# Performance work log

Hardware: AMD Instinct MI355X
Metric: run time of the kernel (lower is better)

The kernel has to match this reference:

```python
import jax, jax.numpy as jnp
import numpy as np

NUM_ORI = 16
DEGREE = 2
NUM_LAYERS = 2
LN_EPS = 1e-6


def ori_grid_s1(n):
    theta = jnp.linspace(0.0, 2.0 * jnp.pi, n + 1)[:-1]
    return jnp.stack([jnp.cos(theta), jnp.sin(theta)], axis=-1)  # (O, 2)


def poly_feats(z, degree):
    # PolynomialFeatures: [z, z*z outer, (z*z)*z outer ...] flattened
    feats = [z]
    p = z
    for _ in range(degree):
        p = (p[..., :, None] * z[..., None, :]).reshape(*z.shape[:-1], -1)
        feats.append(p)
    return jnp.concatenate(feats, axis=-1)


def basis_mlp(z, W1, b1, W2, b2):
    return jax.nn.gelu(jax.nn.gelu(z @ W1 + b1) @ W2 + b2)


def layer_norm(h, scale, bias):
    mu = h.mean(axis=-1, keepdims=True)
    var = ((h - mu) ** 2).mean(axis=-1, keepdims=True)
    return (h - mu) * jax.lax.rsqrt(var + LN_EPS) * scale + bias


def setup_inputs() -> dict:
    key = jax.random.key(0)
    ks = jax.random.split(key, 16)
    B, N, NIN, H, BD, WF, OUT, L = 1, 256, 3, 64, 32, 4, 3, NUM_LAYERS
    s = 0.05
    return {
        'pos': jax.random.normal(ks[0], (B, N, 2), jnp.float32),
        'x': jax.random.normal(ks[1], (B, N, NIN), jnp.float32),
        'skb_W1': jax.random.normal(ks[2], (14, H), jnp.float32) * s,
        'skb_b1': jnp.zeros((H,), jnp.float32),
        'skb_W2': jax.random.normal(ks[3], (H, BD), jnp.float32) * s,
        'skb_b2': jnp.zeros((BD,), jnp.float32),
        'rkb_W1': jax.random.normal(ks[4], (3, H), jnp.float32) * s,
        'rkb_b1': jnp.zeros((H,), jnp.float32),
        'rkb_W2': jax.random.normal(ks[5], (H, BD), jnp.float32) * s,
        'rkb_b2': jnp.zeros((BD,), jnp.float32),
        'emb_W': jax.random.normal(ks[6], (NIN, H), jnp.float32) * s,
        'conv_sW': jax.random.normal(ks[7], (L, BD, H), jnp.float32) * s,
        'conv_rW': jax.random.normal(ks[8], (L, BD, H), jnp.float32) * s,
        'conv_b': jnp.zeros((L, H), jnp.float32),
        'ln_scale': jnp.ones((L, H), jnp.float32),
        'ln_bias': jnp.zeros((L, H), jnp.float32),
        'lin1_W': jax.random.normal(ks[9], (L, H, WF * H), jnp.float32) * s,
        'lin1_b': jnp.zeros((L, WF * H), jnp.float32),
        'lin2_W': jax.random.normal(ks[10], (L, WF * H, H), jnp.float32) * s,
        'lin2_b': jnp.zeros((L, H), jnp.float32),
        'readout_W': jax.random.normal(ks[11], (H, OUT), jnp.float32) * s,
    }


def reference(pos, x, skb_W1, skb_b1, skb_W2, skb_b2, rkb_W1, rkb_b1, rkb_W2, rkb_b2,
              emb_W, conv_sW, conv_rW, conv_b, ln_scale, ln_bias,
              lin1_W, lin1_b, lin2_W, lin2_b, readout_W):
    ori = ori_grid_s1(NUM_ORI)  # (O, 2)
    # rel_pos: (B, n, m, 1, 2) -> broadcast against ori (O, 2)
    rel_pos = pos[:, None, :, None, :] - pos[:, :, None, None, :]
    inv1 = jnp.sum(rel_pos * ori[None, None, None, :, :], axis=-1, keepdims=True)  # (B,N,N,O,1)
    inv2 = jnp.linalg.norm(rel_pos - rel_pos * inv1, axis=-1, keepdims=True)       # (B,N,N,O,1)
    spatial_inv = jnp.concatenate([inv1, inv2], axis=-1)                            # (B,N,N,O,2)
    orient_inv = jnp.sum(ori[:, None, :] * ori[None, :, :], axis=-1, keepdims=True) # (O,O,1)

    kernel_basis = basis_mlp(poly_feats(spatial_inv, DEGREE), skb_W1, skb_b1, skb_W2, skb_b2)  # (B,N,N,O,BD)
    fiber_basis = basis_mlp(poly_feats(orient_inv, DEGREE), rkb_W1, rkb_b1, rkb_W2, rkb_b2)    # (O,O,BD)

    h = x @ emb_W                                  # (B,N,H)
    O = NUM_ORI
    h = jnp.broadcast_to(h[:, :, None, :], (h.shape[0], h.shape[1], O, h.shape[2]))  # (B,N,O,H)

    for i in range(NUM_LAYERS):
        inp = h
        sk = kernel_basis @ conv_sW[i]             # (B,N,N,O,H)
        rk = fiber_basis @ conv_rW[i]              # (O,O,H)
        c = jnp.einsum('bnoc,bmnoc->bmoc', h, sk)  # spatial aggregation
        c = jnp.einsum('bmoc,poc->bmpc', c, rk)    # orientation mixing
        c = c + conv_b[i]
        c = layer_norm(c, ln_scale[i], ln_bias[i])
        c = jax.nn.gelu(c @ lin1_W[i] + lin1_b[i]) @ lin2_W[i] + lin2_b[i]
        h = inp + c

    readout = h @ readout_W                        # (B,N,O,OUT)
    out_scalar = readout.mean(axis=-2)             # (B,N,OUT)
    out_scalar = jnp.sum(out_scalar, axis=1) / out_scalar.shape[1]  # global pool -> (B,OUT)
    return out_scalar
```

## Files before the change

kernel.cpp:

```cpp
#include <hip/hip_runtime.h>
#include <math.h>

#define NPTS 256
#define NORI 16
#define CH   64
#define BD   32
#define HID  64
#define STEP16 0.39269908169872414f

typedef __bf16 bf16x8 __attribute__((ext_vector_type(8)));
typedef float  f32x4  __attribute__((ext_vector_type(4)));

#define MFMA16(a, b, cc) __builtin_amdgcn_mfma_f32_16x16x32_bf16(a, b, cc, 0, 0, 0)

__device__ __forceinline__ float gelu_f(float x) {
    float x2 = x * x;
    float y2 = x * fmaf(0.07135481627f, x2, 1.5957691216f);
    float e = __expf(y2);
    return x - x * __builtin_amdgcn_rcpf(e + 1.0f);
}

__device__ __forceinline__ unsigned pk2(float x, float y) {
    union { __bf16 h[2]; unsigned u; } r;
    r.h[0] = (__bf16)x; r.h[1] = (__bf16)y;
    return r.u;
}

__device__ __forceinline__ void dev_prep(
    const float* __restrict__ skb_W1, const float* __restrict__ skb_W2,
    const float* __restrict__ conv_sW,
    __bf16* __restrict__ w1T, __bf16* __restrict__ w2T, __bf16* __restrict__ w2Tlo,
    __bf16* __restrict__ sWT, __bf16* __restrict__ sWTlo, int t)
{
    if (t < 64) {
        float f[9];
        f[0] = skb_W1[t];
        f[1] = skb_W1[64 + t];
        f[2] = skb_W1[128 + t];
        f[3] = skb_W1[192 + t] + skb_W1[256 + t];
        f[4] = skb_W1[320 + t];
        f[5] = skb_W1[384 + t];
        f[6] = skb_W1[448 + t] + skb_W1[512 + t] + skb_W1[640 + t];
        f[7] = skb_W1[576 + t] + skb_W1[704 + t] + skb_W1[768 + t];
        f[8] = skb_W1[832 + t];
#pragma unroll
        for (int k = 0; k < 9; ++k) {
            __bf16 hi = (__bf16)f[k];
            w1T[t * 32 + k]      = hi;
            w1T[t * 32 + 9 + k]  = (__bf16)(f[k] - (float)hi);
            w1T[t * 32 + 18 + k] = hi;
        }
#pragma unroll
        for (int k = 27; k < 32; ++k) w1T[t * 32 + k] = (__bf16)0.0f;
    }
    for (int i = t; i < 2048; i += 256) {
        int n = i >> 6, kk = i & 63;
        float v = skb_W2[kk * 32 + n];
        __bf16 hi = (__bf16)v;
        w2T[i]   = hi;
        w2Tlo[i] = (__bf16)(v - (float)hi);
    }
    for (int i = t; i < 4096; i += 256) {
        int ll = i >> 11, chh = (i >> 5) & 63, k = i & 31;
        float v = conv_sW[(ll * 32 + k) * 64 + chh];
        __bf16 hi = (__bf16)v;
        sWT[i]   = hi;
        sWTlo[i] = (__bf16)(v - (float)hi);
    }
}

__device__ __forceinline__ void dev_fiber(
    const float* __restrict__ rkb_W1, const float* __restrict__ rkb_b1,
    const float* __restrict__ rkb_W2, const float* __restrict__ rkb_b2,
    const float* __restrict__ conv_rW, float* __restrict__ rk, int p, int t)
{
    __shared__ float w1L[3 * 64], b1L[64], w2L[64 * 32], b2L[32];
    __shared__ float rwL[2 * 32 * 64];
    __shared__ float t1L[16 * 64];
    __shared__ float fbL[16 * 32];

    if (t < 192) w1L[t] = rkb_W1[t];
    if (t >= 192 && t < 256) b1L[t - 192] = rkb_b1[t - 192];
    for (int i = t; i < 2048; i += 256) w2L[i] = rkb_W2[i];
    if (t < 32) b2L[t] = rkb_b2[t];
    for (int i = t; i < 4096; i += 256) rwL[i] = conv_rW[i];
    __syncthreads();

    const int o = t & 15;
    const float cp = cosf(p * STEP16), sp = sinf(p * STEP16);
    const float co = cosf(o * STEP16), so = sinf(o * STEP16);
    const float s0 = cp * co + sp * so;
    const float m1 = s0 * s0, m2 = m1 * s0;

    {
        const int jg = t >> 4;
#pragma unroll
        for (int u = 0; u < 4; ++u) {
            const int j = jg * 4 + u;
            float a = b1L[j] + s0 * w1L[j] + m1 * w1L[64 + j] + m2 * w1L[128 + j];
            t1L[o * 64 + j] = gelu_f(a);
        }
    }
    __syncthreads();
    {
        const int kg = t >> 4;
#pragma unroll
        for (int kk = 0; kk < 2; ++kk) {
            const int k = kg + kk * 16;
            float a = b2L[k];
#pragma unroll
            for (int j = 0; j < 64; ++j) a += t1L[o * 64 + j] * w2L[j * 32 + k];
            fbL[o * 32 + k] = gelu_f(a);
        }
    }
    __syncthreads();
    {
        const int o2 = t >> 4;
        const int chg = (t & 15) * 4;
#pragma unroll
        for (int l = 0; l < 2; ++l) {
            f32x4 acc = {0.f, 0.f, 0.f, 0.f};
#pragma unroll
            for (int k = 0; k < 32; ++k) {
                const float fv = fbL[o2 * 32 + k];
                const f32x4 rv = *(const f32x4*)(rwL + (l * 32 + k) * 64 + chg);
                acc[0] = fmaf(fv, rv[0], acc[0]);
                acc[1] = fmaf(fv, rv[1], acc[1]);
                acc[2] = fmaf(fv, rv[2], acc[2]);
                acc[3] = fmaf(fv, rv[3], acc[3]);
            }
            *(f32x4*)(rk + (l * 256 + p * 16 + o2) * 64 + chg) = acc;
        }
    }
}

__global__ __launch_bounds__(256) void k_prep(
    const float* __restrict__ skb_W1, const float* __restrict__ skb_W2,
    const float* __restrict__ conv_sW,
    __bf16* __restrict__ w1T, __bf16* __restrict__ w2T, __bf16* __restrict__ w2Tlo,
    __bf16* __restrict__ sWT, __bf16* __restrict__ sWTlo)
{
    dev_prep(skb_W1, skb_W2, conv_sW, w1T, w2T, w2Tlo, sWT, sWTlo, threadIdx.x);
}

__global__ __launch_bounds__(256) void k_fiber2(
    const float* __restrict__ rkb_W1, const float* __restrict__ rkb_b1,
    const float* __restrict__ rkb_W2, const float* __restrict__ rkb_b2,
    const float* __restrict__ conv_rW, float* __restrict__ rk)
{
    dev_fiber(rkb_W1, rkb_b1, rkb_W2, rkb_b2, conv_rW, rk, blockIdx.x, threadIdx.x);
}

__global__ __launch_bounds__(256) void k_init(
    const float* __restrict__ x, const float* __restrict__ emb_W, float* __restrict__ h)
{
    int idx = blockIdx.x * 256 + threadIdx.x;
    int ch = idx & 63;
    int n  = idx >> 10;
    h[idx] = x[n * 3] * emb_W[ch] + x[n * 3 + 1] * emb_W[64 + ch] + x[n * 3 + 2] * emb_W[128 + ch];
}

__global__ __launch_bounds__(256) void k_setup(
    const float* __restrict__ x, const float* __restrict__ emb_W, float* __restrict__ h2,
    const float* __restrict__ rkb_W1, const float* __restrict__ rkb_b1,
    const float* __restrict__ rkb_W2, const float* __restrict__ rkb_b2,
    const float* __restrict__ conv_rW, float* __restrict__ rk,
    const float* __restrict__ skb_W1, const float* __restrict__ skb_W2,
    const float* __restrict__ conv_sW,
    __bf16* __restrict__ w1T, __bf16* __restrict__ w2T, __bf16* __restrict__ w2Tlo,
    __bf16* __restrict__ sWT, __bf16* __restrict__ sWTlo)
{
    const int b = blockIdx.x, t = threadIdx.x;
    if (b < 1024) {
        int idx = b * 256 + t;
        int ch = (idx >> 4) & 63;
        int n  = idx >> 10;
        h2[idx] = x[n * 3] * emb_W[ch] + x[n * 3 + 1] * emb_W[64 + ch]
                + x[n * 3 + 2] * emb_W[128 + ch];
    } else if (b < 1040) {
        dev_fiber(rkb_W1, rkb_b1, rkb_W2, rkb_b2, conv_rW, rk, b - 1024, t);
    } else {
        dev_prep(skb_W1, skb_W2, conv_sW, w1T, w2T, w2Tlo, sWT, sWTlo, t);
    }
}

__global__ __launch_bounds__(256) void k_kb2(
    const float* __restrict__ pos,
    const float* __restrict__ skb_b1, const float* __restrict__ skb_b2,
    const __bf16* __restrict__ w1T, const __bf16* __restrict__ w2T,
    const __bf16* __restrict__ w2Tlo, __bf16* __restrict__ kb_g)
{
    const int t = threadIdx.x;
    const int c = t & 15, qq = (t >> 4) & 3, w = t >> 6;
    const int pair = blockIdx.x >> 1, ohalf = blockIdx.x & 1;
    const int m0 = (pair >> 4) * 16, n0 = (pair & 15) * 16;

    bf16x8 w1B[4], w2A[2][2], w2Alo[2][2];
    float b1x[4][4], b2x[2][4];
#pragma unroll
    for (int ni = 0; ni < 4; ++ni) {
        w1B[ni] = *(const bf16x8*)(w1T + (ni * 16 + c) * 32 + qq * 8);
#pragma unroll
        for (int r = 0; r < 4; ++r) b1x[ni][r] = skb_b1[ni * 16 + qq * 4 + r];
    }
#pragma unroll
    for (int mk = 0; mk < 2; ++mk) {
#pragma unroll
        for (int ks = 0; ks < 2; ++ks) {
            w2A[mk][ks]   = *(const bf16x8*)(w2T   + (mk * 16 + c) * 64 + ks * 32 + qq * 8);
            w2Alo[mk][ks] = *(const bf16x8*)(w2Tlo + (mk * 16 + c) * 64 + ks * 32 + qq * 8);
        }
#pragma unroll
        for (int r = 0; r < 4; ++r) b2x[mk][r] = skb_b2[mk * 16 + qq * 4 + r];
    }

    const int n = n0 + c;
    const float pnx = pos[2 * n], pny = pos[2 * n + 1];
    float cosv[4], sinv[4];
#pragma unroll
    for (int oi = 0; oi < 4; ++oi) {
        float th = (float)(ohalf * 4 + oi) * STEP16;
        cosv[oi] = cosf(th); sinv[oi] = sinf(th);
    }
    const int s0lane = c + ((qq & 1) << 5);
    const int s1lane = s0lane + 16;
    const int selhi = qq >> 1;
    const f32x4 zf = {0.f, 0.f, 0.f, 0.f};

#pragma unroll 1
    for (int mi = 0; mi < 4; ++mi) {
        const int m = m0 + w * 4 + mi;
        const float dx = pnx - pos[2 * m];
        const float dy = pny - pos[2 * m + 1];
#pragma unroll
        for (int oi = 0; oi < 4; ++oi) {
            const int o = ohalf * 4 + oi;
            float a = dx * cosv[oi] + dy * sinv[oi];
            float vx = dx - dx * a, vy = dy - dy * a;
            float b = sqrtf(vx * vx + vy * vy);
            float mfv[9];
            mfv[0] = a; mfv[1] = b; mfv[2] = a * a; mfv[3] = a * b; mfv[4] = b * b;
            mfv[5] = mfv[2] * a; mfv[6] = mfv[2] * b; mfv[7] = mfv[3] * b; mfv[8] = mfv[4] * b;
            __bf16 mh[9], ml[9];
#pragma unroll
            for (int i = 0; i < 9; ++i) {
                mh[i] = (__bf16)mfv[i];
                ml[i] = (__bf16)(mfv[i] - (float)mh[i]);
            }
            bf16x8 mb;
            if (qq == 0) {
                mb[0]=mh[0]; mb[1]=mh[1]; mb[2]=mh[2]; mb[3]=mh[3];
                mb[4]=mh[4]; mb[5]=mh[5]; mb[6]=mh[6]; mb[7]=mh[7];
            } else if (qq == 1) {
                mb[0]=mh[8]; mb[1]=mh[0]; mb[2]=mh[1]; mb[3]=mh[2];
                mb[4]=mh[3]; mb[5]=mh[4]; mb[6]=mh[5]; mb[7]=mh[6];
            } else if (qq == 2) {
                mb[0]=mh[7]; mb[1]=mh[8]; mb[2]=ml[0]; mb[3]=ml[1];
                mb[4]=ml[2]; mb[5]=ml[3]; mb[6]=ml[4]; mb[7]=ml[5];
            } else {
                mb[0]=ml[6]; mb[1]=ml[7]; mb[2]=ml[8]; mb[3]=(__bf16)0.0f;
                mb[4]=(__bf16)0.0f; mb[5]=(__bf16)0.0f; mb[6]=(__bf16)0.0f; mb[7]=(__bf16)0.0f;
            }

            unsigned t1p[4][2];
#pragma unroll
            for (int ni = 0; ni < 4; ++ni) {
                f32x4 acc = MFMA16(w1B[ni], mb, zf);
                float g0 = gelu_f(acc[0] + b1x[ni][0]);
                float g1 = gelu_f(acc[1] + b1x[ni][1]);
                float g2 = gelu_f(acc[2] + b1x[ni][2]);
                float g3 = gelu_f(acc[3] + b1x[ni][3]);
                t1p[ni][0] = pk2(g0, g1);
                t1p[ni][1] = pk2(g2, g3);
            }

            bf16x8 B2[2];
#pragma unroll
            for (int ks = 0; ks < 2; ++ks) {
                const unsigned lo0 = t1p[ks * 2][0],     lo1 = t1p[ks * 2][1];
                const unsigned hi0 = t1p[ks * 2 + 1][0], hi1 = t1p[ks * 2 + 1][1];
                unsigned aL0 = (unsigned)__shfl((int)lo0, s0lane);
                unsigned aL1 = (unsigned)__shfl((int)lo1, s0lane);
                unsigned aL2 = (unsigned)__shfl((int)lo0, s1lane);
                unsigned aL3 = (unsigned)__shfl((int)lo1, s1lane);
                unsigned aH0 = (unsigned)__shfl((int)hi0, s0lane);
                unsigned aH1 = (unsigned)__shfl((int)hi1, s0lane);
                unsigned aH2 = (unsigned)__shfl((int)hi0, s1lane);
                unsigned aH3 = (unsigned)__shfl((int)hi1, s1lane);
                union { unsigned u[4]; bf16x8 v; } bu;
                bu.u[0] = selhi ? aH0 : aL0;
                bu.u[1] = selhi ? aH1 : aL1;
                bu.u[2] = selhi ? aH2 : aL2;
                bu.u[3] = selhi ? aH3 : aL3;
                B2[ks] = bu.v;
            }

            const size_t ptP = (size_t)((m * 256 + n) * 16 + o);
            const size_t ptM = (size_t)((n * 256 + m) * 16 + (o ^ 8));
#pragma unroll
            for (int mk = 0; mk < 2; ++mk) {
                f32x4 acc = MFMA16(w2A[mk][0], B2[0], zf);
                acc = MFMA16(w2A[mk][1], B2[1], acc);
                acc = MFMA16(w2Alo[mk][0], B2[0], acc);
                acc = MFMA16(w2Alo[mk][1], B2[1], acc);
                float g0 = gelu_f(acc[0] + b2x[mk][0]);
                float g1 = gelu_f(acc[1] + b2x[mk][1]);
                float g2 = gelu_f(acc[2] + b2x[mk][2]);
                float g3 = gelu_f(acc[3] + b2x[mk][3]);
                uint2 pv; pv.x = pk2(g0, g1); pv.y = pk2(g2, g3);
                const int off = mk * 32 + qq * 8;
                *(uint2*)((char*)kb_g + ptP * 64 + off) = pv;
                *(uint2*)((char*)kb_g + ptM * 64 + off) = pv;
            }
        }
    }
}

__global__ __launch_bounds__(1024) void k_conv2(
    const __bf16* __restrict__ kb_g,
    const __bf16* __restrict__ sWT, const __bf16* __restrict__ sWTlo,
    const float* __restrict__ conv_b, const float* __restrict__ rkg,
    const float* __restrict__ ln_scale, const float* __restrict__ ln_bias,
    const float* __restrict__ lin1_W, const float* __restrict__ lin1_b,
    const float* __restrict__ lin2_W, const float* __restrict__ lin2_b,
    const float* __restrict__ h_in, float* __restrict__ h_out, int l)
{
    __shared__ __align__(16) unsigned char smem[90112];
    const int t = threadIdx.x;
    const int m = blockIdx.x;
    const int w = t >> 6, lane = t & 63;
    const int qq = lane >> 4, c = lane & 15;
    const f32x4 zf = {0.f, 0.f, 0.f, 0.f};

    bf16x8 sWB[4], sWBlo[4];
#pragma unroll
    for (int ni = 0; ni < 4; ++ni) {
        sWB[ni]   = *(const bf16x8*)(sWT   + l * 2048 + (ni * 16 + c) * 32 + qq * 8);
        sWBlo[ni] = *(const bf16x8*)(sWTlo + l * 2048 + (ni * 16 + c) * 32 + qq * 8);
    }

    f32x4 cacc[4];
#pragma unroll
    for (int ni = 0; ni < 4; ++ni)
#pragma unroll
        for (int r = 0; r < 4; ++r) cacc[ni][r] = 0.f;

    const __bf16* kbm = kb_g + ((size_t)m << 17);
    const __bf16* abase = kbm + (size_t)(w * 16 + c) * 32 + qq * 8;

    bf16x8 aF = *(const bf16x8*)(abase);
    f32x4 hc0, hc1, hc2, hc3;
    {
        const float* hp = h_in + (w) * 1024 + c * 16 + qq * 4;
        hc0 = *(const f32x4*)(hp);
        hc1 = *(const f32x4*)(hp + 256);
        hc2 = *(const f32x4*)(hp + 512);
        hc3 = *(const f32x4*)(hp + 768);
    }

#pragma unroll 1
    for (int tile = 0; tile < 16; ++tile) {
        const int tn = (tile < 15) ? tile + 1 : 15;
        bf16x8 aN = *(const bf16x8*)(abase + (size_t)tn * 8192);
        const float* hpn = h_in + (tn * 16 + w) * 1024 + c * 16 + qq * 4;
        f32x4 hn0 = *(const f32x4*)(hpn);
        f32x4 hn1 = *(const f32x4*)(hpn + 256);
        f32x4 hn2 = *(const f32x4*)(hpn + 512);
        f32x4 hn3 = *(const f32x4*)(hpn + 768);

        f32x4 g;
        g = MFMA16(aF, sWB[0], zf);
        g = MFMA16(aF, sWBlo[0], g);
#pragma unroll
        for (int r = 0; r < 4; ++r) cacc[0][r] = fmaf(g[r], hc0[r], cacc[0][r]);
        g = MFMA16(aF, sWB[1], zf);
        g = MFMA16(aF, sWBlo[1], g);
#pragma unroll
        for (int r = 0; r < 4; ++r) cacc[1][r] = fmaf(g[r], hc1[r], cacc[1][r]);
        g = MFMA16(aF, sWB[2], zf);
        g = MFMA16(aF, sWBlo[2], g);
#pragma unroll
        for (int r = 0; r < 4; ++r) cacc[2][r] = fmaf(g[r], hc2[r], cacc[2][r]);
        g = MFMA16(aF, sWB[3], zf);
        g = MFMA16(aF, sWBlo[3], g);
#pragma unroll
        for (int r = 0; r < 4; ++r) cacc[3][r] = fmaf(g[r], hc3[r], cacc[3][r]);

        aF = aN;
        hc0 = hn0; hc1 = hn1; hc2 = hn2; hc3 = hn3;
    }

    {
        float* c1p = (float*)smem;
#pragma unroll
        for (int ni = 0; ni < 4; ++ni)
#pragma unroll
            for (int r = 0; r < 4; ++r)
                c1p[w * 1024 + (qq * 4 + r) * 64 + ni * 16 + c] = cacc[ni][r];
    }
    __syncthreads();
    {
        float* c1p = (float*)smem;
        float* c1r = (float*)(smem + 65536);
        float s = 0.f;
#pragma unroll
        for (int ww = 0; ww < 16; ++ww) s += c1p[ww * 1024 + t];
        c1r[t] = s;
    }
    __syncthreads();

    {
        float* c1r = (float*)(smem + 65536);
        float* cns = (float*)(smem + 69632);
        const int ch = lane;
        const float cb  = conv_b[l * 64 + ch];
        const float lsc = ln_scale[l * 64 + ch], lbi = ln_bias[l * 64 + ch];
        const float* rkp = rkg + (l * 256 + w * 16) * 64 + ch;
        float s = cb;
#pragma unroll
        for (int o = 0; o < 16; ++o) s += c1r[o * 64 + ch] * rkp[o * 64];
        float red = s;
#pragma unroll
        for (int off = 32; off > 0; off >>= 1) red += __shfl_xor(red, off);
        float mu = red * (1.0f / 64.0f);
        float d = s - mu;
        float r2 = d * d;
#pragma unroll
        for (int off = 32; off > 0; off >>= 1) r2 += __shfl_xor(r2, off);
        cns[w * 64 + ch] = d * rsqrtf(r2 * (1.0f / 64.0f) + 1e-6f) * lsc + lbi;
    }
    __syncthreads();

    {
        float* cns = (float*)(smem + 69632);
        float* usS = (float*)(smem + 73728);
        const int j = t & 255, q4 = t >> 8;
        const float* W1l = lin1_W + l * 64 * 256;
        const float bl1 = lin1_b[l * 256 + j];
        float ua[4];
#pragma unroll
        for (int pi = 0; pi < 4; ++pi) ua[pi] = bl1;
#pragma unroll 4
        for (int c2 = 0; c2 < 64; ++c2) {
            const float wv = W1l[c2 * 256 + j];
#pragma unroll
            for (int pi = 0; pi < 4; ++pi)
                ua[pi] = fmaf(cns[(q4 * 4 + pi) * 64 + c2], wv, ua[pi]);
        }
#pragma unroll
        for (int pi = 0; pi < 4; ++pi) usS[(q4 * 4 + pi) * 256 + j] = gelu_f(ua[pi]);
    }
    __syncthreads();

    {
        float* usS = (float*)(smem + 73728);
        const int ch2 = t & 63, pg = t >> 6;
        const float* W2l = lin2_W + l * 256 * 64;
        float o0 = lin2_b[l * 64 + ch2];
#pragma unroll 4
        for (int j = 0; j < 256; ++j)
            o0 = fmaf(usS[pg * 256 + j], W2l[j * 64 + ch2], o0);
        const int i0 = m * 1024 + ch2 * 16 + pg;
        h_out[i0] = h_in[i0] + o0;
    }
}

__global__ __launch_bounds__(512, 1) void k_layer2(
    const float* __restrict__ pos,
    const float* __restrict__ skb_b1, const float* __restrict__ skb_b2,
    const __bf16* __restrict__ w1T, const __bf16* __restrict__ w2T,
    const __bf16* __restrict__ w2Tlo,
    const __bf16* __restrict__ sWT, const __bf16* __restrict__ sWTlo,
    const float* __restrict__ conv_b, const float* __restrict__ rkg,
    const float* __restrict__ ln_scale, const float* __restrict__ ln_bias,
    const float* __restrict__ lin1_W, const float* __restrict__ lin1_b,
    const float* __restrict__ lin2_W, const float* __restrict__ lin2_b,
    const float* __restrict__ h_in, float* __restrict__ h_out, int l)
{
    __shared__ __align__(16) unsigned char smem[57344];
    const int t = threadIdx.x;
    const int m = blockIdx.x;
    const int w = t >> 6, lane = t & 63;
    const int qq = lane >> 4, c = lane & 15;

    bf16x8 w1B[4], sWB[4], sWBlo[4], w2B[2][2], w2Blo[2][2];
    float b1v[4], b2v[2];
#pragma unroll
    for (int ni = 0; ni < 4; ++ni) {
        w1B[ni]   = *(const bf16x8*)(w1T + (ni * 16 + c) * 32 + qq * 8);
        sWB[ni]   = *(const bf16x8*)(sWT   + l * 2048 + (ni * 16 + c) * 32 + qq * 8);
        sWBlo[ni] = *(const bf16x8*)(sWTlo + l * 2048 + (ni * 16 + c) * 32 + qq * 8);
        b1v[ni] = skb_b1[ni * 16 + c];
    }
#pragma unroll
    for (int nt = 0; nt < 2; ++nt) {
        b2v[nt] = skb_b2[nt * 16 + c];
#pragma unroll
        for (int ks = 0; ks < 2; ++ks) {
            w2B[nt][ks]   = *(const bf16x8*)(w2T   + (nt * 16 + c) * 64 + ks * 32 + qq * 8);
            w2Blo[nt][ks] = *(const bf16x8*)(w2Tlo + (nt * 16 + c) * 64 + ks * 32 + qq * 8);
        }
    }

    const float pmx = pos[2 * m], pmy = pos[2 * m + 1];
    float co_ = 0.f, so_ = 0.f;
    if (t < 256) { float th = (float)(t & 15) * STEP16; co_ = cosf(th); so_ = sinf(th); }

    f32x4 cacc[4];
#pragma unroll
    for (int ni = 0; ni < 4; ++ni)
#pragma unroll
        for (int r = 0; r < 4; ++r) cacc[ni][r] = 0.f;

#pragma unroll 1
    for (int tile = 0; tile < 16; ++tile) {
        if (t < 256) {
            const int n = tile * 16 + (t >> 4);
            float dx = pos[2 * n] - pmx, dy = pos[2 * n + 1] - pmy;
            float a = dx * co_ + dy * so_;
            float vx = dx - dx * a, vy = dy - dy * a;
            float b = sqrtf(vx * vx + vy * vy);
            float mf[9];
            mf[0] = a; mf[1] = b; mf[2] = a * a; mf[3] = a * b; mf[4] = b * b;
            mf[5] = mf[2] * a; mf[6] = mf[2] * b; mf[7] = mf[3] * b; mf[8] = mf[4] * b;
            __bf16 s[32];
#pragma unroll
            for (int i = 0; i < 9; ++i) {
                __bf16 hi = (__bf16)mf[i];
                s[i] = hi; s[9 + i] = hi;
                s[18 + i] = (__bf16)(mf[i] - (float)hi);
            }
#pragma unroll
            for (int i = 27; i < 32; ++i) s[i] = (__bf16)0.0f;
            unsigned char* rowp = smem + t * 64;
#pragma unroll
            for (int u = 0; u < 4; ++u) {
                bf16x8 vv;
#pragma unroll
                for (int j = 0; j < 8; ++j) vv[j] = s[u * 8 + j];
                *(bf16x8*)(rowp + ((u ^ (t & 3)) << 4)) = vv;
            }
        }
        __syncthreads();

#pragma unroll
        for (int mm = 0; mm < 2; ++mm) {
            const int row = (2 * w + mm) * 16 + c;
            bf16x8 aF = *(const bf16x8*)(smem + row * 64 + ((qq ^ (row & 3)) << 4));
#pragma unroll
            for (int ni = 0; ni < 4; ++ni) {
                f32x4 acc = {0.f, 0.f, 0.f, 0.f};
                acc = MFMA16(aF, w1B[ni], acc);
#pragma unroll
                for (int r = 0; r < 4; ++r) {
                    const int ro = (2 * w + mm) * 16 + qq * 4 + r;
                    float g = gelu_f(acc[r] + b1v[ni]);
                    const int chc = ni * 16 + c;
                    *(__bf16*)(smem + 16384 + ro * 128 + (((chc >> 3) ^ (ro & 7)) << 4)
                               + ((chc & 7) << 1)) = (__bf16)g;
                }
            }
        }
        __syncthreads();

#pragma unroll
        for (int mm = 0; mm < 2; ++mm) {
            const int row = (2 * w + mm) * 16 + c;
            bf16x8 a0 = *(const bf16x8*)(smem + 16384 + row * 128 + ((qq ^ (row & 7)) << 4));
            bf16x8 a1 = *(const bf16x8*)(smem + 16384 + row * 128 + (((4 + qq) ^ (row & 7)) << 4));
#pragma unroll
            for (int nt = 0; nt < 2; ++nt) {
                f32x4 acc = {0.f, 0.f, 0.f, 0.f};
                acc = MFMA16(a0, w2B[nt][0], acc);
                acc = MFMA16(a1, w2B[nt][1], acc);
                acc = MFMA16(a0, w2Blo[nt][0], acc);
                acc = MFMA16(a1, w2Blo[nt][1], acc);
#pragma unroll
                for (int r = 0; r < 4; ++r) {
                    const int ro = (2 * w + mm) * 16 + qq * 4 + r;
                    float g = gelu_f(acc[r] + b2v[nt]);
                    const int kc = nt * 16 + c;
                    *(__bf16*)(smem + ro * 64 + (((kc >> 3) ^ (ro & 3)) << 4)
                               + ((kc & 7) << 1)) = (__bf16)g;
                }
            }
        }
        __syncthreads();

#pragma unroll
        for (int mm = 0; mm < 2; ++mm) {
            const int mi = 2 * w + mm;
            const int row = mi * 16 + c;
            bf16x8 aF = *(const bf16x8*)(smem + row * 64 + ((qq ^ (row & 3)) << 4));
            const int nbase = (tile * 16 + mi) * 1024 + qq * 256;
#pragma unroll
            for (int ni = 0; ni < 4; ++ni) {
                f32x4 g3 = {0.f, 0.f, 0.f, 0.f};
                g3 = MFMA16(aF, sWB[ni], g3);
                g3 = MFMA16(aF, sWBlo[ni], g3);
#pragma unroll
                for (int r = 0; r < 4; ++r) {
                    float hv = h_in[nbase + r * 64 + ni * 16 + c];
                    cacc[ni][r] = fmaf(g3[r], hv, cacc[ni][r]);
                }
            }
        }
        __syncthreads();
    }

    {
        float* c1p = (float*)smem;
#pragma unroll
        for (int ni = 0; ni < 4; ++ni)
#pragma unroll
            for (int r = 0; r < 4; ++r)
                c1p[w * 1024 + (qq * 4 + r) * 64 + ni * 16 + c] = cacc[ni][r];
    }
    __syncthreads();
    {
        float* c1p = (float*)smem;
        float* c1r = (float*)(smem + 32768);
        for (int i = t; i < 1024; i += 512) {
            float s = 0.f;
#pragma unroll
            for (int ww = 0; ww < 8; ++ww) s += c1p[ww * 1024 + i];
            c1r[i] = s;
        }
    }
    __syncthreads();

    {
        float* c1r = (float*)(smem + 32768);
        float* cns = (float*)(smem + 36864);
        const int ch = lane;
        const float cb  = conv_b[l * 64 + ch];
        const float lsc = ln_scale[l * 64 + ch], lbi = ln_bias[l * 64 + ch];
#pragma unroll
        for (int pp = 0; pp < 2; ++pp) {
            const int p = w + pp * 8;
            const float* rkp = rkg + (l * 256 + p * 16) * 64 + ch;
            float s = cb;
#pragma unroll
            for (int o = 0; o < 16; ++o) s += c1r[o * 64 + ch] * rkp[o * 64];
            float red = s;
#pragma unroll
            for (int off = 32; off > 0; off >>= 1) red += __shfl_xor(red, off);
            float mu = red * (1.0f / 64.0f);
            float d = s - mu;
            float r2 = d * d;
#pragma unroll
            for (int off = 32; off > 0; off >>= 1) r2 += __shfl_xor(r2, off);
            cns[p * 64 + ch] = d * rsqrtf(r2 * (1.0f / 64.0f) + 1e-6f) * lsc + lbi;
        }
    }
    __syncthreads();

    {
        float* cns = (float*)(smem + 36864);
        float* usS = (float*)(smem + 40960);
        const int j = t & 255, half = t >> 8;
        const float* W1l = lin1_W + l * 64 * 256;
        const float bl1 = lin1_b[l * 256 + j];
        float ua[8];
#pragma unroll
        for (int pi = 0; pi < 8; ++pi) ua[pi] = bl1;
#pragma unroll 1
        for (int c2 = 0; c2 < 64; ++c2) {
            const float wv = W1l[c2 * 256 + j];
#pragma unroll
            for (int pi = 0; pi < 8; ++pi)
                ua[pi] = fmaf(cns[(half * 8 + pi) * 64 + c2], wv, ua[pi]);
        }
#pragma unroll
        for (int pi = 0; pi < 8; ++pi) usS[(half * 8 + pi) * 256 + j] = gelu_f(ua[pi]);
    }
    __syncthreads();

    {
        float* usS = (float*)(smem + 40960);
        const int ch2 = t & 63, pg = t >> 6;
        const float* W2l = lin2_W + l * 256 * 64;
        const float bl2 = lin2_b[l * 64 + ch2];
        float o0 = bl2, o1 = bl2;
#pragma unroll 2
        for (int j = 0; j < 256; ++j) {
            const float wv = W2l[j * 64 + ch2];
            o0 = fmaf(usS[pg * 256 + j], wv, o0);
            o1 = fmaf(usS[(pg + 8) * 256 + j], wv, o1);
        }
        const int i0 = (m * 16 + pg) * 64 + ch2;
        const int i1 = (m * 16 + pg + 8) * 64 + ch2;
        h_out[i0] = h_in[i0] + o0;
        h_out[i1] = h_in[i1] + o1;
    }
}

__global__ __launch_bounds__(256) void k_readout_part(
    const float* __restrict__ h, float* __restrict__ part16)
{
    __shared__ float part[4][64];
    const int t = threadIdx.x, b = blockIdx.x;
    const int c = t & 63, seg = t >> 6;
    float s = 0.f;
    const int r0 = b * 256 + seg * 64;
    for (int r = r0; r < r0 + 64; ++r) s += h[r * 64 + c];
    part[seg][c] = s;
    __syncthreads();
    if (t < 64) part16[b * 64 + t] = part[0][t] + part[1][t] + part[2][t] + part[3][t];
}

__global__ __launch_bounds__(256) void k_readout_part2(
    const float* __restrict__ h, float* __restrict__ part16)
{
    const int t = threadIdx.x, b = blockIdx.x;
    const int ch = t >> 2, oq = t & 3;
    float s = 0.f;
#pragma unroll
    for (int nn = 0; nn < 16; ++nn) {
        const int n = b * 16 + nn;
        f32x4 v = *(const f32x4*)(h + n * 1024 + ch * 16 + oq * 4);
        s += (v[0] + v[1]) + (v[2] + v[3]);
    }
    s += __shfl_xor(s, 1);
    s += __shfl_xor(s, 2);
    if (oq == 0) part16[b * 64 + ch] = s;
}

__global__ __launch_bounds__(64) void k_readout_final(
    const float* __restrict__ part16, const float* __restrict__ rW, float* __restrict__ out)
{
    __shared__ float hbar[64];
    const int t = threadIdx.x;
    float s = 0.f;
#pragma unroll
    for (int b = 0; b < 16; ++b) s += part16[b * 64 + t];
    hbar[t] = s * (1.0f / 4096.0f);
    __syncthreads();
    if (t < 3) {
        float s2 = 0.f;
#pragma unroll
        for (int k = 0; k < 64; ++k) s2 += hbar[k] * rW[k * 3 + t];
        out[t] = s2;
    }
}

extern "C" void kernel_launch(void* const* d_in, const int* in_sizes, int n_in,
                              void* d_out, int out_size, void* d_ws, size_t ws_size,
                              hipStream_t stream)
{
    const float* pos      = (const float*)d_in[0];
    const float* x        = (const float*)d_in[1];
    const float* skb_W1   = (const float*)d_in[2];
    const float* skb_b1   = (const float*)d_in[3];
    const float* skb_W2   = (const float*)d_in[4];
    const float* skb_b2   = (const float*)d_in[5];
    const float* rkb_W1   = (const float*)d_in[6];
    const float* rkb_b1   = (const float*)d_in[7];
    const float* rkb_W2   = (const float*)d_in[8];
    const float* rkb_b2   = (const float*)d_in[9];
    const float* emb_W    = (const float*)d_in[10];
    const float* conv_sW  = (const float*)d_in[11];
    const float* conv_rW  = (const float*)d_in[12];
    const float* conv_b   = (const float*)d_in[13];
    const float* ln_scale = (const float*)d_in[14];
    const float* ln_bias  = (const float*)d_in[15];
    const float* lin1_W   = (const float*)d_in[16];
    const float* lin1_b   = (const float*)d_in[17];
    const float* lin2_W   = (const float*)d_in[18];
    const float* lin2_b   = (const float*)d_in[19];
    const float* readout_W= (const float*)d_in[20];
    float* out = (float*)d_out;

    unsigned char* ws = (unsigned char*)d_ws;
    float*  h_a    = (float*)(ws);
    float*  h_b    = (float*)(ws + 1048576);
    float*  rkw    = (float*)(ws + 2097152);
    __bf16* w1T    = (__bf16*)(ws + 2228224);
    __bf16* w2T    = (__bf16*)(ws + 2232320);
    __bf16* w2Tlo  = (__bf16*)(ws + 2236416);
    __bf16* sWT    = (__bf16*)(ws + 2240512);
    __bf16* sWTlo  = (__bf16*)(ws + 2248704);
    float*  part16 = (float*)(ws + 2256896);
    __bf16* kb_g   = (__bf16*)(ws + 2260992);

    const bool fast = (ws_size >= 2260992ull + 67108864ull);

    if (fast) {
        k_setup<<<1041, 256, 0, stream>>>(x, emb_W, h_a,
                                          rkb_W1, rkb_b1, rkb_W2, rkb_b2, conv_rW, rkw,
                                          skb_W1, skb_W2, conv_sW,
                                          w1T, w2T, w2Tlo, sWT, sWTlo);
        k_kb2<<<512, 256, 0, stream>>>(pos, skb_b1, skb_b2, w1T, w2T, w2Tlo, kb_g);
        k_conv2<<<256, 1024, 0, stream>>>(kb_g, sWT, sWTlo, conv_b, rkw,
                                          ln_scale, ln_bias, lin1_W, lin1_b,
                                          lin2_W, lin2_b, h_a, h_b, 0);
        k_conv2<<<256, 1024, 0, stream>>>(kb_g, sWT, sWTlo, conv_b, rkw,
                                          ln_scale, ln_bias, lin1_W, lin1_b,
                                          lin2_W, lin2_b, h_b, h_a, 1);
        k_readout_part2<<<16, 256, 0, stream>>>(h_a, part16);
        k_readout_final<<<1, 64, 0, stream>>>(part16, readout_W, out);
    } else {
        k_prep<<<1, 256, 0, stream>>>(skb_W1, skb_W2, conv_sW, w1T, w2T, w2Tlo, sWT, sWTlo);
        k_fiber2<<<16, 256, 0, stream>>>(rkb_W1, rkb_b1, rkb_W2, rkb_b2, conv_rW, rkw);
        k_init<<<1024, 256, 0, stream>>>(x, emb_W, h_a);
        k_layer2<<<256, 512, 0, stream>>>(pos, skb_b1, skb_b2, w1T, w2T, w2Tlo, sWT, sWTlo,
                                          conv_b, rkw, ln_scale, ln_bias, lin1_W, lin1_b,
                                          lin2_W, lin2_b, h_a, h_b, 0);
        k_layer2<<<256, 512, 0, stream>>>(pos, skb_b1, skb_b2, w1T, w2T, w2Tlo, sWT, sWTlo,
                                          conv_b, rkw, ln_scale, ln_bias, lin1_W, lin1_b,
                                          lin2_W, lin2_b, h_b, h_a, 1);
        k_readout_part<<<16, 256, 0, stream>>>(h_a, part16);
        k_readout_final<<<1, 64, 0, stream>>>(part16, readout_W, out);
    }
}
```

Baseline: 146.3 us.

## Stage kernel-basis tiles into LDS via async global_load_lds with swizzled layout

The conv kernel now streams each 16KB kernel-basis tile into a double-buffered LDS region with async global-to-LDS loads and reads MFMA operands from LDS, synchronising once per tile. The kernel-basis producer writes its output with an XOR swizzle on 16-byte chunks so the LDS reads avoid bank conflicts. It also splits the m range across twice as many blocks for more parallelism. The cost is an extra block-wide barrier per tile and a layout coupling between producer and consumer.

```diff
diff --git a/kernel.cpp b/kernel.cpp
--- a/kernel.cpp
+++ b/kernel.cpp
@@ -12,6 +12,9 @@
 typedef float  f32x4  __attribute__((ext_vector_type(4)));
 
 #define MFMA16(a, b, cc) __builtin_amdgcn_mfma_f32_16x16x32_bf16(a, b, cc, 0, 0, 0)
+#define GLOAD_LDS16(g, l) \
+    __builtin_amdgcn_global_load_lds((const __attribute__((address_space(1))) unsigned int*)(g), \
+                                     (__attribute__((address_space(3))) unsigned int*)(l), 16, 0, 0)
 
 __device__ __forceinline__ float gelu_f(float x) {
     float x2 = x * x;
@@ -192,7 +195,10 @@
 {
     const int t = threadIdx.x;
     const int c = t & 15, qq = (t >> 4) & 3, w = t >> 6;
-    const int pair = blockIdx.x >> 1, ohalf = blockIdx.x & 1;
+    const int b = blockIdx.x;
+    const int pair = b >> 2;
+    const int ohalf = (b >> 1) & 1;
+    const int mhalf = b & 1;
     const int m0 = (pair >> 4) * 16, n0 = (pair & 15) * 16;
 
     bf16x8 w1B[4], w2A[2][2], w2Alo[2][2];
@@ -228,8 +234,8 @@
     const f32x4 zf = {0.f, 0.f, 0.f, 0.f};
 
 #pragma unroll 1
-    for (int mi = 0; mi < 4; ++mi) {
-        const int m = m0 + w * 4 + mi;
+    for (int mi2 = 0; mi2 < 2; ++mi2) {
+        const int m = m0 + w * 4 + mhalf * 2 + mi2;
         const float dx = pnx - pos[2 * m];
         const float dy = pny - pos[2 * m + 1];
 #pragma unroll
@@ -237,10 +243,10 @@
             const int o = ohalf * 4 + oi;
             float a = dx * cosv[oi] + dy * sinv[oi];
             float vx = dx - dx * a, vy = dy - dy * a;
-            float b = sqrtf(vx * vx + vy * vy);
+            float b2 = sqrtf(vx * vx + vy * vy);
             float mfv[9];
-            mfv[0] = a; mfv[1] = b; mfv[2] = a * a; mfv[3] = a * b; mfv[4] = b * b;
-            mfv[5] = mfv[2] * a; mfv[6] = mfv[2] * b; mfv[7] = mfv[3] * b; mfv[8] = mfv[4] * b;
+            mfv[0] = a; mfv[1] = b2; mfv[2] = a * a; mfv[3] = a * b2; mfv[4] = b2 * b2;
+            mfv[5] = mfv[2] * a; mfv[6] = mfv[2] * b2; mfv[7] = mfv[3] * b2; mfv[8] = mfv[4] * b2;
             __bf16 mh[9], ml[9];
 #pragma unroll
             for (int i = 0; i < 9; ++i) {
@@ -297,6 +303,7 @@
 
             const size_t ptP = (size_t)((m * 256 + n) * 16 + o);
             const size_t ptM = (size_t)((n * 256 + m) * 16 + (o ^ 8));
+            const int swz = o & 3;
 #pragma unroll
             for (int mk = 0; mk < 2; ++mk) {
                 f32x4 acc = MFMA16(w2A[mk][0], B2[0], zf);
@@ -308,7 +315,7 @@
                 float g2 = gelu_f(acc[2] + b2x[mk][2]);
                 float g3 = gelu_f(acc[3] + b2x[mk][3]);
                 uint2 pv; pv.x = pk2(g0, g1); pv.y = pk2(g2, g3);
-                const int off = mk * 32 + qq * 8;
+                const int off = (((mk * 2 + (qq >> 1)) ^ swz) << 4) + ((qq & 1) << 3);
                 *(uint2*)((char*)kb_g + ptP * 64 + off) = pv;
                 *(uint2*)((char*)kb_g + ptM * 64 + off) = pv;
             }
@@ -316,7 +323,7 @@
     }
 }
 
-__global__ __launch_bounds__(1024) void k_conv2(
+__global__ __launch_bounds__(1024) void k_conv3(
     const __bf16* __restrict__ kb_g,
     const __bf16* __restrict__ sWT, const __bf16* __restrict__ sWTlo,
     const float* __restrict__ conv_b, const float* __restrict__ rkg,
@@ -345,29 +352,34 @@
 #pragma unroll
         for (int r = 0; r < 4; ++r) cacc[ni][r] = 0.f;
 
-    const __bf16* kbm = kb_g + ((size_t)m << 17);
-    const __bf16* abase = kbm + (size_t)(w * 16 + c) * 32 + qq * 8;
-
-    bf16x8 aF = *(const bf16x8*)(abase);
+    const char* kbm = (const char*)kb_g + (size_t)m * 262144;
+    const char* gsrc0 = kbm + w * 1024 + lane * 16;
+    char* lbase = (char*)smem + w * 1024;
+
+    GLOAD_LDS16(gsrc0, lbase);
     f32x4 hc0, hc1, hc2, hc3;
     {
-        const float* hp = h_in + (w) * 1024 + c * 16 + qq * 4;
+        const float* hp = h_in + w * 1024 + c * 16 + qq * 4;
         hc0 = *(const f32x4*)(hp);
         hc1 = *(const f32x4*)(hp + 256);
         hc2 = *(const f32x4*)(hp + 512);
         hc3 = *(const f32x4*)(hp + 768);
     }
-
-#pragma unroll 1
+    __syncthreads();
+
+#pragma unroll 2
     for (int tile = 0; tile < 16; ++tile) {
+        const int bufoff = (tile & 1) << 14;
+        if (tile < 15)
+            GLOAD_LDS16(gsrc0 + (size_t)(tile + 1) * 16384, lbase + (bufoff ^ 16384));
         const int tn = (tile < 15) ? tile + 1 : 15;
-        bf16x8 aN = *(const bf16x8*)(abase + (size_t)tn * 8192);
         const float* hpn = h_in + (tn * 16 + w) * 1024 + c * 16 + qq * 4;
         f32x4 hn0 = *(const f32x4*)(hpn);
         f32x4 hn1 = *(const f32x4*)(hpn + 256);
         f32x4 hn2 = *(const f32x4*)(hpn + 512);
         f32x4 hn3 = *(const f32x4*)(hpn + 768);
 
+        bf16x8 aF = *(const bf16x8*)(smem + bufoff + (w * 16 + c) * 64 + ((qq ^ (c & 3)) << 4));
         f32x4 g;
         g = MFMA16(aF, sWB[0], zf);
         g = MFMA16(aF, sWBlo[0], g);
@@ -386,7 +398,7 @@
 #pragma unroll
         for (int r = 0; r < 4; ++r) cacc[3][r] = fmaf(g[r], hc3[r], cacc[3][r]);
 
-        aF = aN;
+        __syncthreads();
         hc0 = hn0; hc1 = hn1; hc2 = hn2; hc3 = hn3;
     }
 
@@ -790,11 +802,11 @@
                                           rkb_W1, rkb_b1, rkb_W2, rkb_b2, conv_rW, rkw,
                                           skb_W1, skb_W2, conv_sW,
                                           w1T, w2T, w2Tlo, sWT, sWTlo);
-        k_kb2<<<512, 256, 0, stream>>>(pos, skb_b1, skb_b2, w1T, w2T, w2Tlo, kb_g);
-        k_conv2<<<256, 1024, 0, stream>>>(kb_g, sWT, sWTlo, conv_b, rkw,
+        k_kb2<<<1024, 256, 0, stream>>>(pos, skb_b1, skb_b2, w1T, w2T, w2Tlo, kb_g);
+        k_conv3<<<256, 1024, 0, stream>>>(kb_g, sWT, sWTlo, conv_b, rkw,
                                           ln_scale, ln_bias, lin1_W, lin1_b,
                                           lin2_W, lin2_b, h_a, h_b, 0);
-        k_conv2<<<256, 1024, 0, stream>>>(kb_g, sWT, sWTlo, conv_b, rkw,
+        k_conv3<<<256, 1024, 0, stream>>>(kb_g, sWT, sWTlo, conv_b, rkw,
                                           ln_scale, ln_bias, lin1_W, lin1_b,
                                           lin2_W, lin2_b, h_b, h_a, 1);
         k_readout_part2<<<16, 256, 0, stream>>>(h_a, part16);
```

Measured after the change: 157.2 us. +7.4%, slower.
